# Kernel optimization log

Measured on AMD Instinct MI355X. Metric: run time of the kernel, lower is better.

## Reference

```python
import jax, jax.numpy as jnp
import numpy as np

N_NODES = 50000
N_EDGES = 800000
D_IN = 128
D_OUT = 128


def setup_inputs() -> dict:
    key = jax.random.key(0)
    k1, k2, k3, k4, k5 = jax.random.split(key, 5)
    x = jax.random.normal(k1, (N_NODES, D_IN), dtype=jnp.float32)
    edge_index = jax.random.randint(k2, (2, N_EDGES), 0, N_NODES, dtype=jnp.int64)
    scale = 1.0 / np.sqrt(D_IN)
    W_rel = jax.random.normal(k3, (D_OUT, D_IN), dtype=jnp.float32) * scale
    b_rel = jax.random.normal(k4, (D_OUT,), dtype=jnp.float32) * scale
    W_root = jax.random.normal(k5, (D_OUT, D_IN), dtype=jnp.float32) * scale
    return {"x": x, "edge_index": edge_index, "W_rel": W_rel, "b_rel": b_rel, "W_root": W_root}


def reference(x, edge_index, W_rel, b_rel, W_root):
    # PyG GraphConv (aggr='add'):
    #   out_i = W_rel @ (sum_{j->i} x_j) + b_rel + W_root @ x_i
    # followed by ReLU (normalization=None, dropout=0 -> identity).
    src = edge_index[0]  # message source j
    dst = edge_index[1]  # message target i
    n = x.shape[0]
    agg = jax.ops.segment_sum(x[src], dst, num_segments=n)  # [N, D_IN]
    out = agg @ W_rel.T + b_rel + x @ W_root.T              # [N, D_OUT]
    return jax.nn.relu(out)
```

## Files before the change

### kernel.cpp

```cpp
#include <hip/hip_runtime.h>
#include <hip/hip_bf16.h>


#define N_NODES 50000
#define N_EDGES 800000
#define D 128
#define SLOTS 48
#define NB 782
#define TILES 3125
#define BCAP 1536
#define BINB 196
#define NPB 32
#define KC 32
#define SROW 136
#define DUMMY 50000

#define CVT_N  (N_NODES * (D / 2))
#define PACK_N (8 * 8 * 64 * 8)
#define ZROW_N (D / 2)

typedef __attribute__((ext_vector_type(8))) short short8;
typedef __attribute__((ext_vector_type(4))) float floatx4;

__device__ __forceinline__ float bf2f(unsigned short u) {
    return __uint_as_float((unsigned int)u << 16);
}
__device__ __forceinline__ unsigned short f2bf(float f) {
    __hip_bfloat16 h = __float2bfloat16(f);
    return *(unsigned short*)&h;
}

__device__ __forceinline__ int wave_detect_i64(const int* __restrict__ ei) {
    int lane = threadIdx.x & 63;
    int v = ei[2 * lane + 1];
    return __ballot(v == 0) == ~0ull;
}

__global__ __launch_bounds__(256) void zero_f4_kernel(float4* __restrict__ p, int n4) {
    int i = blockIdx.x * 256 + threadIdx.x;
    if (i < n4) p[i] = make_float4(0.f, 0.f, 0.f, 0.f);
}

__global__ void detect_kernel(const int* __restrict__ ei, int* __restrict__ flag) {
    if (threadIdx.x == 0 && blockIdx.x == 0) {
        int any = 0;
        for (int i = 0; i < 64; ++i) any |= ei[2 * i + 1];
        flag[0] = (any == 0) ? 1 : 0;
    }
}

__global__ __launch_bounds__(256) void stage1_kernel(const float2* __restrict__ x2,
                                                     ushort2* __restrict__ xb2,
                                                     const float* __restrict__ Wrel,
                                                     const float* __restrict__ Wroot,
                                                     unsigned short* __restrict__ pwc,
                                                     const int* __restrict__ ei,
                                                     int* __restrict__ gcur,
                                                     unsigned* __restrict__ bmem,
                                                     int* __restrict__ ovf_cnt,
                                                     int* __restrict__ ovf) {
    __shared__ int lds_cnt[NB];
    __shared__ int lds_base[NB];
    if (blockIdx.x < BINB) {
        int t = threadIdx.x;
        int i64 = wave_detect_i64(ei);
        for (int i = t; i < NB; i += 256) lds_cnt[i] = 0;
        __syncthreads();

        unsigned rec[16];
        int rnk[16];
#pragma unroll
        for (int g = 0; g < 4; ++g) {
            int base = blockIdx.x * 4096 + g * 1024 + t * 4;
            int s0 = -1, s1 = -1, s2 = -1, s3 = -1;
            int d0 = -1, d1 = -1, d2 = -1, d3 = -1;
            if (base < N_EDGES) {
                if (i64) {
                    int4 a = *(const int4*)&ei[2 * base];
                    int4 b = *(const int4*)&ei[2 * base + 4];
                    s0 = a.x; s1 = a.z; s2 = b.x; s3 = b.z;
                    int4 c = *(const int4*)&ei[2 * N_EDGES + 2 * base];
                    int4 e = *(const int4*)&ei[2 * N_EDGES + 2 * base + 4];
                    d0 = c.x; d1 = c.z; d2 = e.x; d3 = e.z;
                } else {
                    int4 sv = *(const int4*)&ei[base];
                    int4 dv = *(const int4*)&ei[N_EDGES + base];
                    s0 = sv.x; s1 = sv.y; s2 = sv.z; s3 = sv.w;
                    d0 = dv.x; d1 = dv.y; d2 = dv.z; d3 = dv.w;
                }
            }
#define BINP(idx, ss, dd)                                                        \
            {                                                                    \
                bool ok = (unsigned)(ss) < N_NODES && (unsigned)(dd) < N_NODES;  \
                rec[idx] = ok ? (((unsigned)(dd) << 16) | (unsigned)(ss))        \
                              : 0xFFFFFFFFu;                                     \
                rnk[idx] = ok ? atomicAdd(&lds_cnt[(unsigned)(dd) >> 6], 1) : 0; \
            }
            BINP(g * 4 + 0, s0, d0)
            BINP(g * 4 + 1, s1, d1)
            BINP(g * 4 + 2, s2, d2)
            BINP(g * 4 + 3, s3, d3)
#undef BINP
        }
        __syncthreads();
        for (int i = t; i < NB; i += 256) {
            int c = lds_cnt[i];
            lds_base[i] = c ? atomicAdd(&gcur[i], c) : 0;
        }
        __syncthreads();
#pragma unroll
        for (int idx = 0; idx < 16; ++idx) {
            unsigned r = rec[idx];
            if (r != 0xFFFFFFFFu) {
                int bk = (int)(r >> 22);
                int pos = lds_base[bk] + rnk[idx];
                if (pos < BCAP) {
                    bmem[(size_t)bk * BCAP + pos] = r;
                } else {
                    int o = atomicAdd(ovf_cnt, 1);
                    ovf[2 * o] = (int)(r >> 16);
                    ovf[2 * o + 1] = (int)(r & 0xFFFFu);
                }
            }
        }
    } else {
        int i = (blockIdx.x - BINB) * 256 + threadIdx.x;
        if (i < CVT_N) {
            float2 f = x2[i];
            xb2[i] = make_ushort2(f2bf(f.x), f2bf(f.y));
        } else if (i < CVT_N + PACK_N) {
            int idx  = i - CVT_N;
            int j    = idx & 7;
            int lane = (idx >> 3) & 63;
            int n0   = (idx >> 9) & 7;
            int t    = idx >> 12;
            int n = n0 * 16 + (lane & 15);
            int k = t * 32 + (lane >> 4) * 8 + j;
            float w = (k < D) ? Wrel[n * D + k] : Wroot[n * D + (k - D)];
            pwc[idx] = f2bf(w);
        } else if (i < CVT_N + PACK_N + ZROW_N) {
            xb2[CVT_N + (i - CVT_N - PACK_N)] = make_ushort2(0, 0);
        }
    }
}

__global__ __launch_bounds__(256, 8) void GraphConvLayer_55783035240593_kernel(
        const ushort2* __restrict__ xb2,
        const unsigned short* __restrict__ xb,
        const int* __restrict__ gcur,
        const unsigned* __restrict__ bmem,
        const int* __restrict__ ovf_cnt,
        const int* __restrict__ ovf,
        const unsigned short* __restrict__ pwc,
        const float* __restrict__ b_rel,
        float* __restrict__ out) {
    __shared__ unsigned short sA[16 * SROW];
    __shared__ unsigned short slotsL[16 * SLOTS];
    __shared__ int lc[16];
    int t = threadIdx.x;
    int wid = t >> 6, lane = t & 63;
    int tile = blockIdx.x;
    int bkt = tile >> 2;
    unsigned q = (unsigned)(tile & 3);
    int node0 = tile * 16;

    int n = gcur[bkt];
    int tov = ovf_cnt[0];
    if (t < 16) lc[t] = 0;
    for (int i = t; i < 16 * SLOTS / 2; i += 256)
        ((unsigned*)slotsL)[i] = (DUMMY << 16) | DUMMY;
    __syncthreads();

    if (n > BCAP) n = BCAP;
    for (int e = t; e < n; e += 256) {
        unsigned r = bmem[(size_t)bkt * BCAP + e];
        if (((r >> 20) & 3u) != q) continue;
        int dl = (int)((r >> 16) & 15);
        int p = atomicAdd(&lc[dl], 1);
        if (p < SLOTS) slotsL[dl * SLOTS + p] = (unsigned short)(r & 0xFFFFu);
    }
    __syncthreads();

    int kk0 = lc[wid * 4 + 0], kk1 = lc[wid * 4 + 1];
    int kk2 = lc[wid * 4 + 2], kk3 = lc[wid * 4 + 3];
    int kc0 = (kk0 > SLOTS) ? 0 : kk0;
    int kc1 = (kk1 > SLOTS) ? 0 : kk1;
    int kc2 = (kk2 > SLOTS) ? 0 : kk2;
    int kc3 = (kk3 > SLOTS) ? 0 : kk3;
    int sl = lane < SLOTS ? lane : 0;
    int my0 = (kk0 > SLOTS) ? DUMMY : (int)slotsL[(wid * 4 + 0) * SLOTS + sl];
    int my1 = (kk1 > SLOTS) ? DUMMY : (int)slotsL[(wid * 4 + 1) * SLOTS + sl];
    int my2 = (kk2 > SLOTS) ? DUMMY : (int)slotsL[(wid * 4 + 2) * SLOTS + sl];
    int my3 = (kk3 > SLOTS) ? DUMMY : (int)slotsL[(wid * 4 + 3) * SLOTS + sl];
    int jmax = kc0 > kc1 ? kc0 : kc1;
    jmax = kc2 > jmax ? kc2 : jmax;
    jmax = kc3 > jmax ? kc3 : jmax;
    float ax0 = 0.f, ay0 = 0.f, ax1 = 0.f, ay1 = 0.f;
    float ax2 = 0.f, ay2 = 0.f, ax3 = 0.f, ay3 = 0.f;
    for (int j = 0; j < jmax; j += 8) {
        ushort2 u0[8], u1[8], u2[8], u3[8];
#pragma unroll
        for (int v = 0; v < 8; ++v) {
            int s = __shfl(my0, j + v);
            u0[v] = xb2[(size_t)s * (D / 2) + lane];
        }
#pragma unroll
        for (int v = 0; v < 8; ++v) {
            int s = __shfl(my1, j + v);
            u1[v] = xb2[(size_t)s * (D / 2) + lane];
        }
#pragma unroll
        for (int v = 0; v < 8; ++v) {
            int s = __shfl(my2, j + v);
            u2[v] = xb2[(size_t)s * (D / 2) + lane];
        }
#pragma unroll
        for (int v = 0; v < 8; ++v) {
            int s = __shfl(my3, j + v);
            u3[v] = xb2[(size_t)s * (D / 2) + lane];
        }
#pragma unroll
        for (int v = 0; v < 8; ++v) { ax0 += bf2f(u0[v].x); ay0 += bf2f(u0[v].y); }
#pragma unroll
        for (int v = 0; v < 8; ++v) { ax1 += bf2f(u1[v].x); ay1 += bf2f(u1[v].y); }
#pragma unroll
        for (int v = 0; v < 8; ++v) { ax2 += bf2f(u2[v].x); ay2 += bf2f(u2[v].y); }
#pragma unroll
        for (int v = 0; v < 8; ++v) { ax3 += bf2f(u3[v].x); ay3 += bf2f(u3[v].y); }
    }

    int nodeb = node0 + wid * 4;
    if (kk0 > SLOTS || kk1 > SLOTS || kk2 > SLOTS || kk3 > SLOTS) {
        for (int e = 0; e < n; ++e) {
            unsigned r = bmem[(size_t)bkt * BCAP + e];
            int dd = (int)(r >> 16);
            ushort2 uu;
            if (kk0 > SLOTS && dd == nodeb + 0) {
                uu = xb2[(size_t)(r & 0xFFFFu) * (D / 2) + lane];
                ax0 += bf2f(uu.x); ay0 += bf2f(uu.y);
            } else if (kk1 > SLOTS && dd == nodeb + 1) {
                uu = xb2[(size_t)(r & 0xFFFFu) * (D / 2) + lane];
                ax1 += bf2f(uu.x); ay1 += bf2f(uu.y);
            } else if (kk2 > SLOTS && dd == nodeb + 2) {
                uu = xb2[(size_t)(r & 0xFFFFu) * (D / 2) + lane];
                ax2 += bf2f(uu.x); ay2 += bf2f(uu.y);
            } else if (kk3 > SLOTS && dd == nodeb + 3) {
                uu = xb2[(size_t)(r & 0xFFFFu) * (D / 2) + lane];
                ax3 += bf2f(uu.x); ay3 += bf2f(uu.y);
            }
        }
    }
    if (tov > 0) {
        for (int e2 = 0; e2 < tov; ++e2) {
            int dd = ovf[2 * e2];
            int rel = dd - nodeb;
            if ((unsigned)rel < 4u) {
                ushort2 uu = xb2[(size_t)ovf[2 * e2 + 1] * (D / 2) + lane];
                if (rel == 0)      { ax0 += bf2f(uu.x); ay0 += bf2f(uu.y); }
                else if (rel == 1) { ax1 += bf2f(uu.x); ay1 += bf2f(uu.y); }
                else if (rel == 2) { ax2 += bf2f(uu.x); ay2 += bf2f(uu.y); }
                else               { ax3 += bf2f(uu.x); ay3 += bf2f(uu.y); }
            }
        }
    }
    *(ushort2*)&sA[(wid * 4 + 0) * SROW + 2 * lane] = make_ushort2(f2bf(ax0), f2bf(ay0));
    *(ushort2*)&sA[(wid * 4 + 1) * SROW + 2 * lane] = make_ushort2(f2bf(ax1), f2bf(ay1));
    *(ushort2*)&sA[(wid * 4 + 2) * SROW + 2 * lane] = make_ushort2(f2bf(ax2), f2bf(ay2));
    *(ushort2*)&sA[(wid * 4 + 3) * SROW + 2 * lane] = make_ushort2(f2bf(ax3), f2bf(ay3));
    __syncthreads();

    int m = lane & 15, quad = lane >> 4;
    const unsigned short* arow = &sA[m * SROW + quad * 8];
    const unsigned short* xrow = xb + (size_t)(node0 + m) * D + quad * 8;

    floatx4 acc0 = (floatx4){0.f, 0.f, 0.f, 0.f};
    floatx4 acc1 = (floatx4){0.f, 0.f, 0.f, 0.f};
#pragma unroll
    for (int tt = 0; tt < 8; ++tt) {
        short8 afrag = (tt < 4) ? *(const short8*)(arow + tt * 32)
                                : *(const short8*)(xrow + (tt - 4) * 32);
        const unsigned short* bb = pwc + ((size_t)(tt * 8 + wid * 2) * 64 + lane) * 8;
        short8 b0 = *(const short8*)bb;
        short8 b1 = *(const short8*)(bb + 64 * 8);
        acc0 = __builtin_amdgcn_mfma_f32_16x16x32_bf16(afrag, b0, acc0, 0, 0, 0);
        acc1 = __builtin_amdgcn_mfma_f32_16x16x32_bf16(afrag, b1, acc1, 0, 0, 0);
    }

#pragma unroll
    for (int qq = 0; qq < 2; ++qq) {
        floatx4 a = qq ? acc1 : acc0;
        int nn = (wid * 2 + qq) * 16 + m;
        float bias = b_rel[nn];
#pragma unroll
        for (int r = 0; r < 4; ++r) {
            int node = node0 + quad * 4 + r;
            out[(size_t)node * D + nn] = fmaxf(a[r] + bias, 0.f);
        }
    }
}

__global__ __launch_bounds__(256) void pack_w_kernel(const float* __restrict__ W,
                                                     float* __restrict__ pw) {
    int idx = blockIdx.x * 256 + threadIdx.x;
    if (idx >= D * D) return;
    int o = idx >> 7, k = idx & 127;
    pw[k * D + o] = W[o * D + k];
}

__global__ __launch_bounds__(256) void hist_kernel(const int* __restrict__ ei,
                                                   int* __restrict__ deg) {
    int i64 = wave_detect_i64(ei);
    int base = (blockIdx.x * 256 + threadIdx.x) * 4;
    if (base >= N_EDGES) return;
    int d0, d1, d2, d3;
    if (i64) {
        int4 a = *(const int4*)&ei[2 * N_EDGES + 2 * base];
        int4 b = *(const int4*)&ei[2 * N_EDGES + 2 * base + 4];
        d0 = a.x; d1 = a.z; d2 = b.x; d3 = b.z;
    } else {
        int4 v = *(const int4*)&ei[N_EDGES + base];
        d0 = v.x; d1 = v.y; d2 = v.z; d3 = v.w;
    }
    if ((unsigned)d0 < N_NODES) atomicAdd(&deg[d0], 1);
    if ((unsigned)d1 < N_NODES) atomicAdd(&deg[d1], 1);
    if ((unsigned)d2 < N_NODES) atomicAdd(&deg[d2], 1);
    if ((unsigned)d3 < N_NODES) atomicAdd(&deg[d3], 1);
}

__device__ __forceinline__ int wave_iscan(int v, int lane) {
#pragma unroll
    for (int off = 1; off < 64; off <<= 1) {
        int u = __shfl_up(v, off, 64);
        if (lane >= off) v += u;
    }
    return v;
}

__global__ __launch_bounds__(1024) void scan_kernel(const int* __restrict__ deg,
                                                    int* __restrict__ offsets,
                                                    int* __restrict__ cursor) {
    __shared__ int wsum[16];
    __shared__ int base_s;
    int t = threadIdx.x, lane = t & 63, w = t >> 6;
    if (t == 0) { base_s = 0; offsets[0] = 0; }
    __syncthreads();
    for (int c0 = 0; c0 < N_NODES; c0 += 1024) {
        int idx = c0 + t;
        int v = (idx < N_NODES) ? deg[idx] : 0;
        int inc = wave_iscan(v, lane);
        if (lane == 63) wsum[w] = inc;
        __syncthreads();
        if (w == 0) {
            int s = (lane < 16) ? wsum[lane] : 0;
            int si = wave_iscan(s, lane);
            if (lane < 16) wsum[lane] = si - s;
        }
        __syncthreads();
        int tot = base_s + wsum[w] + inc;
        if (idx < N_NODES) {
            offsets[idx + 1] = tot;
            cursor[idx] = tot - v;
        }
        __syncthreads();
        if (t == 1023) base_s = tot;
        __syncthreads();
    }
}

__global__ __launch_bounds__(256) void reorder_kernel(const int* __restrict__ ei,
                                                      int* __restrict__ cursor,
                                                      int* __restrict__ csr_src) {
    int i64 = wave_detect_i64(ei);
    int base = (blockIdx.x * 256 + threadIdx.x) * 4;
    if (base >= N_EDGES) return;
    int s0, s1, s2, s3, d0, d1, d2, d3;
    if (i64) {
        int4 a = *(const int4*)&ei[2 * base];
        int4 b = *(const int4*)&ei[2 * base + 4];
        s0 = a.x; s1 = a.z; s2 = b.x; s3 = b.z;
        int4 c = *(const int4*)&ei[2 * N_EDGES + 2 * base];
        int4 e = *(const int4*)&ei[2 * N_EDGES + 2 * base + 4];
        d0 = c.x; d1 = c.z; d2 = e.x; d3 = e.z;
    } else {
        int4 sv = *(const int4*)&ei[base];
        int4 dv = *(const int4*)&ei[N_EDGES + base];
        s0 = sv.x; s1 = sv.y; s2 = sv.z; s3 = sv.w;
        d0 = dv.x; d1 = dv.y; d2 = dv.z; d3 = dv.w;
    }
    bool v0 = (unsigned)s0 < N_NODES && (unsigned)d0 < N_NODES;
    bool v1 = (unsigned)s1 < N_NODES && (unsigned)d1 < N_NODES;
    bool v2 = (unsigned)s2 < N_NODES && (unsigned)d2 < N_NODES;
    bool v3 = (unsigned)s3 < N_NODES && (unsigned)d3 < N_NODES;
    int p0 = v0 ? atomicAdd(&cursor[d0], 1) : 0;
    int p1 = v1 ? atomicAdd(&cursor[d1], 1) : 0;
    int p2 = v2 ? atomicAdd(&cursor[d2], 1) : 0;
    int p3 = v3 ? atomicAdd(&cursor[d3], 1) : 0;
    if (v0) csr_src[p0] = s0;
    if (v1) csr_src[p1] = s1;
    if (v2) csr_src[p2] = s2;
    if (v3) csr_src[p3] = s3;
}

__global__ __launch_bounds__(256) void gather_kernel(const float2* __restrict__ x2,
                                                     const int* __restrict__ csr_src,
                                                     const int* __restrict__ offsets,
                                                     float2* __restrict__ agg2) {
    int node = blockIdx.x * 4 + (threadIdx.x >> 6);
    int lane = threadIdx.x & 63;
    if (node >= N_NODES) return;
    int beg = offsets[node], end = offsets[node + 1];
    float2 acc = make_float2(0.f, 0.f);
    for (int e = beg; e < end; ++e) {
        int s = csr_src[e];
        float2 f = x2[(size_t)s * (D / 2) + lane];
        acc.x += f.x;
        acc.y += f.y;
    }
    agg2[(size_t)node * (D / 2) + lane] = acc;
}

__global__ __launch_bounds__(256) void scatter_kernel(const float2* __restrict__ x2,
                                                      const int* __restrict__ ei,
                                                      const int* __restrict__ flag,
                                                      float* __restrict__ agg) {
    int wave = threadIdx.x >> 6;
    int lane = threadIdx.x & 63;
    int e = blockIdx.x * 4 + wave;
    if (e >= N_EDGES) return;
    int i64 = flag ? flag[0] : 0;
    int s, d;
    if (i64) { s = ei[2 * e]; d = ei[2 * N_EDGES + 2 * e]; }
    else     { s = ei[e];     d = ei[N_EDGES + e]; }
    if ((unsigned)s >= N_NODES || (unsigned)d >= N_NODES) return;
    float2 f = x2[(size_t)s * (D / 2) + lane];
    atomicAdd(&agg[(size_t)d * D + 2 * lane + 0], f.x);
    atomicAdd(&agg[(size_t)d * D + 2 * lane + 1], f.y);
}

__global__ __launch_bounds__(256) void gemm_f32_kernel(
        const float2* __restrict__ x2,
        const float* __restrict__ pwrel,
        const float* __restrict__ pwroot,
        const float* __restrict__ b_rel,
        float* __restrict__ out) {
    __shared__ float sWrel[KC * D];
    __shared__ float sWroot[KC * D];
    __shared__ float2 sAm[NPB * (KC / 2)];
    __shared__ float2 sXm[NPB * (KC / 2)];

    int t = threadIdx.x;
    int node0 = blockIdx.x * NPB;
    int tn = t >> 5;
    int to = t & 31;

    float acc[4][4];
#pragma unroll
    for (int a = 0; a < 4; ++a)
#pragma unroll
        for (int b = 0; b < 4; ++b) acc[a][b] = 0.0f;

    for (int c = 0; c < 4; ++c) {
        __syncthreads();
#pragma unroll
        for (int r = 0; r < 4; ++r) {
            int i = r * 256 + t;
            ((float4*)sWrel)[i]  = ((const float4*)(pwrel  + c * KC * D))[i];
            ((float4*)sWroot)[i] = ((const float4*)(pwroot + c * KC * D))[i];
        }
#pragma unroll
        for (int r = 0; r < 2; ++r) {
            int i = r * 256 + t;
            int n = i >> 4, k2 = i & 15;
            int node = node0 + n;
            float2 av = make_float2(0.f, 0.f), xv = make_float2(0.f, 0.f);
            if (node < N_NODES) {
                av = ((const float2*)out)[(size_t)node * (D / 2) + c * (KC / 2) + k2];
                xv = x2[(size_t)node * (D / 2) + c * (KC / 2) + k2];
            }
            sAm[i] = av;
            sXm[i] = xv;
        }
        __syncthreads();

#pragma unroll
        for (int k2 = 0; k2 < KC / 2; ++k2) {
            float4 wr0 = *(const float4*)&sWrel[(2 * k2 + 0) * D + to * 4];
            float4 wr1 = *(const float4*)&sWrel[(2 * k2 + 1) * D + to * 4];
            float4 wt0 = *(const float4*)&sWroot[(2 * k2 + 0) * D + to * 4];
            float4 wt1 = *(const float4*)&sWroot[(2 * k2 + 1) * D + to * 4];
#pragma unroll
            for (int ni = 0; ni < 4; ++ni) {
                float2 a  = sAm[(tn * 4 + ni) * (KC / 2) + k2];
                float2 xx = sXm[(tn * 4 + ni) * (KC / 2) + k2];
                acc[ni][0] += a.x * wr0.x + a.y * wr1.x + xx.x * wt0.x + xx.y * wt1.x;
                acc[ni][1] += a.x * wr0.y + a.y * wr1.y + xx.x * wt0.y + xx.y * wt1.y;
                acc[ni][2] += a.x * wr0.z + a.y * wr1.z + xx.x * wt0.z + xx.y * wt1.z;
                acc[ni][3] += a.x * wr0.w + a.y * wr1.w + xx.x * wt0.w + xx.y * wt1.w;
            }
        }
    }

    int o0 = to * 4;
    float4 bias = *(const float4*)&b_rel[o0];
#pragma unroll
    for (int ni = 0; ni < 4; ++ni) {
        int node = node0 + tn * 4 + ni;
        if (node >= N_NODES) continue;
        float4 v;
        v.x = fmaxf(acc[ni][0] + bias.x, 0.f);
        v.y = fmaxf(acc[ni][1] + bias.y, 0.f);
        v.z = fmaxf(acc[ni][2] + bias.z, 0.f);
        v.w = fmaxf(acc[ni][3] + bias.w, 0.f);
        *(float4*)&out[(size_t)node * D + o0] = v;
    }
}

__global__ __launch_bounds__(128) void gemm_fallback_kernel(const float* __restrict__ x,
                                                            const float* __restrict__ Wrel,
                                                            const float* __restrict__ Wroot,
                                                            const float* __restrict__ b_rel,
                                                            float* __restrict__ out) {
    __shared__ float rowA[D];
    __shared__ float rowX[D];
    int node = blockIdx.x;
    int o = threadIdx.x;
    rowA[o] = out[(size_t)node * D + o];
    rowX[o] = x[(size_t)node * D + o];
    __syncthreads();
    float acc = b_rel[o];
    const float4* wr = (const float4*)&Wrel[o * D];
    const float4* wt = (const float4*)&Wroot[o * D];
#pragma unroll 8
    for (int k4 = 0; k4 < D / 4; ++k4) {
        float4 w = wr[k4], u = wt[k4];
        const float* a = &rowA[k4 * 4];
        const float* xx = &rowX[k4 * 4];
        acc += a[0] * w.x + a[1] * w.y + a[2] * w.z + a[3] * w.w
             + xx[0] * u.x + xx[1] * u.y + xx[2] * u.z + xx[3] * u.w;
    }
    __syncthreads();
    out[(size_t)node * D + o] = fmaxf(acc, 0.f);
}

extern "C" void kernel_launch(void* const* d_in, const int* in_sizes, int n_in,
                              void* d_out, int out_size, void* d_ws, size_t ws_size,
                              hipStream_t stream) {
    const float* x      = (const float*)d_in[0];
    const int*   ei     = (const int*)d_in[1];
    const float* W_rel  = (const float*)d_in[2];
    const float* b_rel  = (const float*)d_in[3];
    const float* W_root = (const float*)d_in[4];
    float*       out    = (float*)d_out;

    char* p = (char*)d_ws;
    size_t o0 = 16;
    int*            flag    = (int*)p;
    unsigned short* pwc     = (unsigned short*)(p + o0);  o0 += (size_t)PACK_N * 2;
    unsigned short* xb      = (unsigned short*)(p + o0);  o0 += (size_t)(N_NODES + 1) * D * 2;
    const size_t gcur_pad = ((size_t)NB * 4 + 15) & ~(size_t)15;
    int*            gcur    = (int*)(p + o0);             o0 += gcur_pad;
    int*            ovf_cnt = (int*)(p + o0);             o0 += 16;
    unsigned*       bmem    = (unsigned*)(p + o0);        o0 += (size_t)NB * BCAP * 4;
    int*            ovf     = (int*)(p + o0);             o0 += (size_t)N_EDGES * 8;
    const size_t need_full = o0;

    size_t m0 = 16;
    float* m_pwrel  = (float*)(p + m0);  m0 += (size_t)D * D * 4;
    float* m_pwroot = (float*)(p + m0);  m0 += (size_t)D * D * 4;
    int*   m_deg    = (int*)(p + m0);    m0 += (size_t)N_NODES * 4;
    int*   m_offs   = (int*)(p + m0);    m0 += ((size_t)N_NODES + 1) * 4 + 12;
    m0 &= ~15ull;
    int*   m_csr    = (int*)(p + m0);    m0 += (size_t)N_EDGES * 4;
    const size_t need_mid = m0;
    const size_t need_pw  = 16 + 2 * (size_t)D * D * 4;

    const int eb4 = (N_EDGES / 4 + 255) / 256;

    if (ws_size >= need_full) {
        hipMemsetAsync(gcur, 0, gcur_pad + 16, stream);
        const int prep_total = CVT_N + PACK_N + ZROW_N;
        const int grid1 = BINB + (prep_total + 255) / 256;
        stage1_kernel<<<grid1, 256, 0, stream>>>(
            (const float2*)x, (ushort2*)xb, W_rel, W_root, pwc, ei,
            gcur, bmem, ovf_cnt, ovf);
        GraphConvLayer_55783035240593_kernel<<<TILES, 256, 0, stream>>>(
            (const ushort2*)xb, xb, gcur, bmem, ovf_cnt, ovf, pwc, b_rel, out);
    } else if (ws_size >= need_mid) {
        pack_w_kernel<<<64, 256, 0, stream>>>(W_rel, m_pwrel);
        pack_w_kernel<<<64, 256, 0, stream>>>(W_root, m_pwroot);
        zero_f4_kernel<<<(N_NODES / 4 + 255) / 256, 256, 0, stream>>>((float4*)m_deg,
                                                                      N_NODES / 4);
        hist_kernel<<<eb4, 256, 0, stream>>>(ei, m_deg);
        scan_kernel<<<1, 1024, 0, stream>>>(m_deg, m_offs, m_deg);
        reorder_kernel<<<eb4, 256, 0, stream>>>(ei, m_deg, m_csr);
        gather_kernel<<<N_NODES / 4, 256, 0, stream>>>((const float2*)x, m_csr,
                                                       m_offs, (float2*)out);
        gemm_f32_kernel<<<(N_NODES + NPB - 1) / NPB, 256, 0, stream>>>(
            (const float2*)x, m_pwrel, m_pwroot, b_rel, out);
    } else {
        bool have_flag = ws_size >= 16;
        bool have_pw   = ws_size >= need_pw;
        if (have_flag) detect_kernel<<<1, 64, 0, stream>>>(ei, flag);
        if (have_pw) {
            pack_w_kernel<<<64, 256, 0, stream>>>(W_rel, m_pwrel);
            pack_w_kernel<<<64, 256, 0, stream>>>(W_root, m_pwroot);
        }
        int n4 = N_NODES * D / 4;
        zero_f4_kernel<<<(n4 + 255) / 256, 256, 0, stream>>>((float4*)out, n4);
        scatter_kernel<<<N_EDGES / 4, 256, 0, stream>>>((const float2*)x, ei,
                                                        have_flag ? flag : nullptr, out);
        if (have_pw)
            gemm_f32_kernel<<<(N_NODES + NPB - 1) / NPB, 256, 0, stream>>>(
                (const float2*)x, m_pwrel, m_pwroot, b_rel, out);
        else
            gemm_fallback_kernel<<<N_NODES, 128, 0, stream>>>(x, W_rel, W_root, b_rel, out);
    }
}
```

Baseline: 147.8 us.

## Gather neighbor rows with 16-byte loads and double-buffer the aggregation loop

The neighbor gather now has each lane load 8 bf16 values (16 bytes) instead of 2, so 16 lanes cover a row and four neighbors are fetched at once per node. The partial sums are then combined across quarter-waves with xor shuffles. Loads for the next group of neighbors are issued before the current group is accumulated (a software double buffer), to overlap gather latency with the adds. The block-to-tile mapping is swizzled to change which tiles run together for cache locality, and occupancy is lowered to 4 blocks per CU to free registers for the extra accumulators. This uses more registers and shuffles and pads the slot index at the end of a node's list, in exchange for fewer, wider memory transactions.

```diff
diff --git a/kernel.cpp b/kernel.cpp
--- a/kernel.cpp
+++ b/kernel.cpp
@@ -20,6 +20,7 @@
 #define ZROW_N (D / 2)
 
 typedef __attribute__((ext_vector_type(8))) short short8;
+typedef __attribute__((ext_vector_type(8))) unsigned short ushort8;
 typedef __attribute__((ext_vector_type(4))) float floatx4;
 
 __device__ __forceinline__ float bf2f(unsigned short u) {
@@ -144,7 +145,7 @@
     }
 }
 
-__global__ __launch_bounds__(256, 8) void GraphConvLayer_55783035240593_kernel(
+__global__ __launch_bounds__(256, 4) void GraphConvLayer_55783035240593_kernel(
         const ushort2* __restrict__ xb2,
         const unsigned short* __restrict__ xb,
         const int* __restrict__ gcur,
@@ -157,9 +158,19 @@
     __shared__ unsigned short sA[16 * SROW];
     __shared__ unsigned short slotsL[16 * SLOTS];
     __shared__ int lc[16];
+    const ushort8* __restrict__ xb8 = (const ushort8*)xb;
     int t = threadIdx.x;
     int wid = t >> 6, lane = t & 63;
-    int tile = blockIdx.x;
+    int qd = lane >> 4, m = lane & 15;
+
+    int blk = blockIdx.x;
+    int tile;
+    if (blk < 3104) {
+        int g = blk >> 5, x = blk & 7, s = (blk >> 3) & 3;
+        tile = ((g << 3) | x) * 4 + s;
+    } else {
+        tile = blk;
+    }
     int bkt = tile >> 2;
     unsigned q = (unsigned)(tile & 3);
     int node0 = tile * 16;
@@ -195,38 +206,35 @@
     int jmax = kc0 > kc1 ? kc0 : kc1;
     jmax = kc2 > jmax ? kc2 : jmax;
     jmax = kc3 > jmax ? kc3 : jmax;
-    float ax0 = 0.f, ay0 = 0.f, ax1 = 0.f, ay1 = 0.f;
-    float ax2 = 0.f, ay2 = 0.f, ax3 = 0.f, ay3 = 0.f;
+
+    float a0[8], a1[8], a2[8], a3[8];
+#pragma unroll
+    for (int e = 0; e < 8; ++e) { a0[e] = 0.f; a1[e] = 0.f; a2[e] = 0.f; a3[e] = 0.f; }
+
+#define LG(BUF, MY, jb) { int ix = (jb) + qd; ix = ix < SLOTS ? ix : SLOTS - 1;   \
+                          int s = __shfl(MY, ix);                                 \
+                          BUF = xb8[(size_t)s * (D / 8) + m]; }
+#define CG(ACC, BUF) { _Pragma("unroll")                                          \
+                       for (int e = 0; e < 8; ++e)                                \
+                           ACC[e] += bf2f((unsigned short)BUF[e]); }
+
+    ushort8 A0, A1, A2, A3, B0, B1, B2, B3;
+    LG(A0, my0, 0) LG(A1, my1, 0) LG(A2, my2, 0) LG(A3, my3, 0)
     for (int j = 0; j < jmax; j += 8) {
-        ushort2 u0[8], u1[8], u2[8], u3[8];
-#pragma unroll
-        for (int v = 0; v < 8; ++v) {
-            int s = __shfl(my0, j + v);
-            u0[v] = xb2[(size_t)s * (D / 2) + lane];
-        }
-#pragma unroll
-        for (int v = 0; v < 8; ++v) {
-            int s = __shfl(my1, j + v);
-            u1[v] = xb2[(size_t)s * (D / 2) + lane];
-        }
-#pragma unroll
-        for (int v = 0; v < 8; ++v) {
-            int s = __shfl(my2, j + v);
-            u2[v] = xb2[(size_t)s * (D / 2) + lane];
-        }
-#pragma unroll
-        for (int v = 0; v < 8; ++v) {
-            int s = __shfl(my3, j + v);
-            u3[v] = xb2[(size_t)s * (D / 2) + lane];
-        }
-#pragma unroll
-        for (int v = 0; v < 8; ++v) { ax0 += bf2f(u0[v].x); ay0 += bf2f(u0[v].y); }
-#pragma unroll
-        for (int v = 0; v < 8; ++v) { ax1 += bf2f(u1[v].x); ay1 += bf2f(u1[v].y); }
-#pragma unroll
-        for (int v = 0; v < 8; ++v) { ax2 += bf2f(u2[v].x); ay2 += bf2f(u2[v].y); }
-#pragma unroll
-        for (int v = 0; v < 8; ++v) { ax3 += bf2f(u3[v].x); ay3 += bf2f(u3[v].y); }
+        LG(B0, my0, j + 4) LG(B1, my1, j + 4) LG(B2, my2, j + 4) LG(B3, my3, j + 4)
+        CG(a0, A0) CG(a1, A1) CG(a2, A2) CG(a3, A3)
+        LG(A0, my0, j + 8) LG(A1, my1, j + 8) LG(A2, my2, j + 8) LG(A3, my3, j + 8)
+        CG(a0, B0) CG(a1, B1) CG(a2, B2) CG(a3, B3)
+    }
+#undef LG
+#undef CG
+
+#pragma unroll
+    for (int e = 0; e < 8; ++e) {
+        a0[e] += __shfl_xor(a0[e], 16); a0[e] += __shfl_xor(a0[e], 32);
+        a1[e] += __shfl_xor(a1[e], 16); a1[e] += __shfl_xor(a1[e], 32);
+        a2[e] += __shfl_xor(a2[e], 16); a2[e] += __shfl_xor(a2[e], 32);
+        a3[e] += __shfl_xor(a3[e], 16); a3[e] += __shfl_xor(a3[e], 32);
     }
 
     int nodeb = node0 + wid * 4;
@@ -234,44 +242,63 @@
         for (int e = 0; e < n; ++e) {
             unsigned r = bmem[(size_t)bkt * BCAP + e];
             int dd = (int)(r >> 16);
-            ushort2 uu;
-            if (kk0 > SLOTS && dd == nodeb + 0) {
-                uu = xb2[(size_t)(r & 0xFFFFu) * (D / 2) + lane];
-                ax0 += bf2f(uu.x); ay0 += bf2f(uu.y);
-            } else if (kk1 > SLOTS && dd == nodeb + 1) {
-                uu = xb2[(size_t)(r & 0xFFFFu) * (D / 2) + lane];
-                ax1 += bf2f(uu.x); ay1 += bf2f(uu.y);
-            } else if (kk2 > SLOTS && dd == nodeb + 2) {
-                uu = xb2[(size_t)(r & 0xFFFFu) * (D / 2) + lane];
-                ax2 += bf2f(uu.x); ay2 += bf2f(uu.y);
-            } else if (kk3 > SLOTS && dd == nodeb + 3) {
-                uu = xb2[(size_t)(r & 0xFFFFu) * (D / 2) + lane];
-                ax3 += bf2f(uu.x); ay3 += bf2f(uu.y);
-            }
-        }
-    }
-    if (tov > 0) {
-        for (int e2 = 0; e2 < tov; ++e2) {
-            int dd = ovf[2 * e2];
             int rel = dd - nodeb;
             if ((unsigned)rel < 4u) {
-                ushort2 uu = xb2[(size_t)ovf[2 * e2 + 1] * (D / 2) + lane];
-                if (rel == 0)      { ax0 += bf2f(uu.x); ay0 += bf2f(uu.y); }
-                else if (rel == 1) { ax1 += bf2f(uu.x); ay1 += bf2f(uu.y); }
-                else if (rel == 2) { ax2 += bf2f(uu.x); ay2 += bf2f(uu.y); }
-                else               { ax3 += bf2f(uu.x); ay3 += bf2f(uu.y); }
+                bool ov = (rel == 0 && kk0 > SLOTS) || (rel == 1 && kk1 > SLOTS) ||
+                          (rel == 2 && kk2 > SLOTS) || (rel == 3 && kk3 > SLOTS);
+                if (ov) {
+                    ushort8 uu = xb8[(size_t)(r & 0xFFFFu) * (D / 8) + m];
+#pragma unroll
+                    for (int e2 = 0; e2 < 8; ++e2) {
+                        float f = bf2f((unsigned short)uu[e2]);
+                        if (rel == 0) a0[e2] += f;
+                        else if (rel == 1) a1[e2] += f;
+                        else if (rel == 2) a2[e2] += f;
+                        else a3[e2] += f;
+                    }
+                }
             }
         }
     }
-    *(ushort2*)&sA[(wid * 4 + 0) * SROW + 2 * lane] = make_ushort2(f2bf(ax0), f2bf(ay0));
-    *(ushort2*)&sA[(wid * 4 + 1) * SROW + 2 * lane] = make_ushort2(f2bf(ax1), f2bf(ay1));
-    *(ushort2*)&sA[(wid * 4 + 2) * SROW + 2 * lane] = make_ushort2(f2bf(ax2), f2bf(ay2));
-    *(ushort2*)&sA[(wid * 4 + 3) * SROW + 2 * lane] = make_ushort2(f2bf(ax3), f2bf(ay3));
+    if (tov > 0) {
+        for (int e = 0; e < tov; ++e) {
+            int dd = ovf[2 * e];
+            int rel = dd - nodeb;
+            if ((unsigned)rel < 4u) {
+                ushort8 uu = xb8[(size_t)ovf[2 * e + 1] * (D / 8) + m];
+#pragma unroll
+                for (int e2 = 0; e2 < 8; ++e2) {
+                    float f = bf2f((unsigned short)uu[e2]);
+                    if (rel == 0) a0[e2] += f;
+                    else if (rel == 1) a1[e2] += f;
+                    else if (rel == 2) a2[e2] += f;
+                    else a3[e2] += f;
+                }
+            }
+        }
+    }
+
+    {
+        ushort8 wv;
+        if (qd == 0) {
+#pragma unroll
+            for (int e = 0; e < 8; ++e) wv[e] = f2bf(a0[e]);
+        } else if (qd == 1) {
+#pragma unroll
+            for (int e = 0; e < 8; ++e) wv[e] = f2bf(a1[e]);
+        } else if (qd == 2) {
+#pragma unroll
+            for (int e = 0; e < 8; ++e) wv[e] = f2bf(a2[e]);
+        } else {
+#pragma unroll
+            for (int e = 0; e < 8; ++e) wv[e] = f2bf(a3[e]);
+        }
+        *(ushort8*)&sA[(wid * 4 + qd) * SROW + 8 * m] = wv;
+    }
     __syncthreads();
 
-    int m = lane & 15, quad = lane >> 4;
-    const unsigned short* arow = &sA[m * SROW + quad * 8];
-    const unsigned short* xrow = xb + (size_t)(node0 + m) * D + quad * 8;
+    const unsigned short* arow = &sA[m * SROW + qd * 8];
+    const unsigned short* xrow = xb + (size_t)(node0 + m) * D + qd * 8;
 
     floatx4 acc0 = (floatx4){0.f, 0.f, 0.f, 0.f};
     floatx4 acc1 = (floatx4){0.f, 0.f, 0.f, 0.f};
@@ -293,7 +320,7 @@
         float bias = b_rel[nn];
 #pragma unroll
         for (int r = 0; r < 4; ++r) {
-            int node = node0 + quad * 4 + r;
+            int node = node0 + qd * 4 + r;
             out[(size_t)node * D + nn] = fmaxf(a[r] + bias, 0.f);
         }
     }
```

Measured after the change: 149.1 us. About the same (+0.8%).
